# Performance work log

Hardware: AMD Instinct MI355X
Metric: run time of the kernel (lower is better)

The kernel has to match this reference:

```python
import jax, jax.numpy as jnp
import numpy as np
import itertools, math

METRIC = [1.0, 1.0, 1.0]  # Cl(3,0)
EPS = 1e-6
SQRT2 = math.sqrt(2.0)


def _build_algebra(metric):
    d = len(metric)
    # basis blades ordered by grade, then lexicographic combination (repo convention)
    blades = []
    for g in range(d + 1):
        for c in itertools.combinations(range(d), g):
            blades.append(sum(1 << i for i in c))
    idx = {m: i for i, m in enumerate(blades)}
    n = len(blades)
    C = np.zeros((n, n, n), dtype=np.float32)  # cayley[i, j, k]: e_i * e_k -> sign * e_j
    for ia, am in enumerate(blades):
        for ik, bm in enumerate(blades):
            a = am >> 1
            swaps = 0
            while a:
                swaps += bin(a & bm).count('1')
                a >>= 1
            sign = -1.0 if (swaps & 1) else 1.0
            for i in range(d):
                if am & bm & (1 << i):
                    sign *= metric[i]
            C[ia, idx[am ^ bm], ik] = sign
    grades = np.array([bin(m).count('1') for m in blades])
    subspaces = np.array([int((grades == g).sum()) for g in range(d + 1)])
    paths = np.zeros((d + 1, d + 1, d + 1), dtype=bool)
    for i in range(d + 1):
        for j in range(d + 1):
            for k in range(d + 1):
                paths[i, j, k] = np.any(C[np.ix_(grades == i, grades == j, grades == k)] != 0)
    return C, subspaces, paths, grades

CAYLEY_NP, SUBSPACES, PATHS, GRADE_OF_COMP = _build_algebra(METRIC)
REP_IDX = np.repeat(np.arange(len(SUBSPACES)), SUBSPACES)  # component -> grade, len 8
PI, PJ, PK = np.nonzero(PATHS)                              # 20 active grade triples
ONEHOT_GRADE = np.eye(len(SUBSPACES), dtype=np.float32)[GRADE_OF_COMP]  # [8,4]

B, N_IN, N_OUT = 1024, 256, 256
DIM_MV = CAYLEY_NP.shape[0]  # 8
N_PATHS = int(PATHS.sum())   # 20


def mv_linear(x, w, bias=None):
    # MVLinear: per-grade weight repeated over components; einsum 'bm...i,nmi->bn...i'
    wr = w[:, :, REP_IDX]                       # [out, in, 8]
    out = jnp.einsum('bmi,nmi->bni', x, wr)
    if bias is not None:
        out = out.at[:, :, 0].add(bias[:, :, 0])  # bias embedded in scalar (grade-0) slot
    return out


def normalize_mv(x, a):
    # per-grade norms (Euclidean metric => L2 norm of each grade block)
    oh = jnp.asarray(ONEHOT_GRADE)
    norms = jnp.sqrt(jnp.einsum('bni,ig->bng', x * x, oh))  # [b, n, 4]
    interp = jax.nn.sigmoid(a)[None] * (norms - 1.0) + 1.0  # learned interp toward unit norm
    return x / (interp[:, :, REP_IDX] + EPS)


def gp_kernel(gp_weight):
    # scatter 20 path weights into (m, n, 4, 4, 4), repeat per subspace, mask by cayley
    m, n, _ = gp_weight.shape
    g = len(SUBSPACES)
    w4 = jnp.zeros((m, n, g, g, g), gp_weight.dtype).at[:, :, PI, PJ, PK].set(gp_weight)
    wrep = w4[:, :, REP_IDX][:, :, :, REP_IDX][:, :, :, :, REP_IDX]  # [m, n, 8, 8, 8]
    return jnp.asarray(CAYLEY_NP)[None, None] * wrep


def setup_inputs() -> dict:
    key = jax.random.key(0)
    ks = jax.random.split(key, 5)
    std_gp = 1.0 / math.sqrt(N_IN * (len(METRIC) + 1))
    std_lin = 1.0 / math.sqrt(N_IN)
    return {
        'x': jax.random.normal(ks[0], (B, N_IN, DIM_MV), jnp.float32),
        'w_right': jax.random.normal(ks[1], (N_IN, N_IN, len(SUBSPACES)), jnp.float32) * std_lin,
        'w_left': jax.random.normal(ks[2], (N_OUT, N_IN, len(SUBSPACES)), jnp.float32) * std_lin,
        'b_left': jax.random.normal(ks[3], (1, N_OUT, 1), jnp.float32) * 0.02,
        'norm_a': jnp.zeros((N_IN, len(SUBSPACES)), jnp.float32),  # normalization_init = 0
        'gp_weight': jax.random.normal(ks[4], (N_OUT, N_IN, N_PATHS), jnp.float32) * std_gp,
    }


def reference(x, w_right, w_left, b_left, norm_a, gp_weight):
    x_right = normalize_mv(mv_linear(x, w_right), norm_a)
    kernel = gp_kernel(gp_weight)                 # [m, n, 8, 8, 8]
    outer = jnp.einsum('bni,bnk->bnik', x, x_right)  # [b, n, 8, 8]
    prod = jnp.einsum('bnik,mnijk->bmj', outer, kernel)
    left = mv_linear(x, w_left, b_left)
    return (left + prod) / SQRT2
```

## Files before the change

### kernel.cpp

```cpp
#include <hip/hip_runtime.h>
#include <math.h>

typedef unsigned short ushortT;
typedef __bf16 bf16x8 __attribute__((ext_vector_type(8)));
typedef float  f32x4  __attribute__((ext_vector_type(4)));

__constant__ int GRADEc[8] = {0,1,1,1,2,2,2,3};

__constant__ int CMAPc[8][7] = {
  {0, 8, 9,10,11, 0, 0},
  {1,12,13,14,15,16,17},
  {2,18,19,20,21,22,23},
  {3,24,25,26,27,28,29},
  {4,30,31,32,33,34,35},
  {5,36,37,38,39,40,41},
  {6,42,43,44,45,46,47},
  {7,48,49,50,51, 0, 0}};
__constant__ int WMAPc[8][7] = {
  {0, 4, 8,14,20, 0, 0},
  {1, 5, 9,10,15,16,21},
  {1, 5, 9,10,15,16,21},
  {1, 5, 9,10,15,16,21},
  {2, 6,11,12,17,18,22},
  {2, 6,11,12,17,18,22},
  {2, 6,11,12,17,18,22},
  {3, 7,13,19,23, 0, 0}};
__constant__ int SSTARTc[8][4] = {
  {0,2,3,4},{0,2,4,6},{0,2,4,6},{0,2,4,6},
  {0,2,4,6},{0,2,4,6},{0,2,4,6},{0,2,3,4}};
__constant__ int SCOUNTc[8][4] = {
  {2,1,1,1},{2,2,2,1},{2,2,2,1},{2,2,2,1},
  {2,2,2,1},{2,2,2,1},{2,2,2,1},{2,1,1,1}};

__device__ __forceinline__ ushortT f2bf(float f) {
  unsigned int u = __float_as_uint(f);
  unsigned int r = (u + 0x7fffu + ((u >> 16) & 1u)) >> 16;
  return (ushortT)r;
}

__global__ void k_transpose_x(const float* __restrict__ x, float* __restrict__ xT) {
  __shared__ float tile[32][33];
  int c0 = blockIdx.x * 32;
  int b0 = blockIdx.y * 32;
  int tx = threadIdx.x & 31, ty = threadIdx.x >> 5;
  #pragma unroll
  for (int i = 0; i < 32; i += 8)
    tile[ty + i][tx] = x[(b0 + ty + i) * 2048 + c0 + tx];
  __syncthreads();
  #pragma unroll
  for (int i = 0; i < 32; i += 8)
    xT[(c0 + ty + i) * 1024 + b0 + tx] = tile[tx][ty + i];
}

__global__ void k_build_wr(const float* __restrict__ w_right, float* __restrict__ WR) {
  int t = blockIdx.x * 256 + threadIdx.x;
  int n = t & 255, m = (t >> 8) & 255, g = t >> 16;
  WR[t] = w_right[n * 1024 + m * 4 + g];
}

__global__ void k_build_wt2(const float* __restrict__ w_left, const float* __restrict__ gp,
                            ushortT* __restrict__ WT2b) {
  int t = blockIdx.x * 256 + threadIdx.x;
  int n = t & 255, m = (t >> 8) & 255, w = t >> 16;
  float v;
  if (w < 4)       v = w_left[m * 1024 + n * 4 + w];
  else             v = gp[m * 5120 + n * 20 + (w - 4)];
  WT2b[t] = f2bf(v);
}

__global__ __launch_bounds__(256) void k_gemm_right2(const float* __restrict__ WR,
                                                     const float* __restrict__ xT,
                                                     float* __restrict__ y2) {
  const int i  = blockIdx.z;
  const int g  = GRADEc[i];
  const int b0 = blockIdx.y * 64;
  const int n0 = blockIdx.x * 64;
  __shared__ float sX[32 * 64];
  __shared__ float sW[32 * 64];
  const int t  = threadIdx.x;
  const int tx = t & 15, ty = t >> 4;
  float acc[4][4] = {};
  const float* Xbase = xT + i * 1024 + b0;
  const float* Wbase = WR + g * 65536 + n0;
  for (int k0 = 0; k0 < 256; k0 += 32) {
    int col = t & 63, krow = t >> 6;
    #pragma unroll
    for (int l = 0; l < 8; ++l) {
      int kk = krow + l * 4;
      sX[kk * 64 + col] = Xbase[(k0 + kk) * 8192 + col];
      sW[kk * 64 + col] = Wbase[(k0 + kk) * 256 + col];
    }
    __syncthreads();
    #pragma unroll
    for (int kk = 0; kk < 32; ++kk) {
      const float4 a = *(const float4*)(sX + kk * 64 + (ty << 2));
      const float4 w = *(const float4*)(sW + kk * 64 + (tx << 2));
      float ar[4] = {a.x, a.y, a.z, a.w};
      float wr4[4] = {w.x, w.y, w.z, w.w};
      #pragma unroll
      for (int r = 0; r < 4; ++r)
        #pragma unroll
        for (int c = 0; c < 4; ++c)
          acc[r][c] = fmaf(ar[r], wr4[c], acc[r][c]);
    }
    __syncthreads();
  }
  #pragma unroll
  for (int r = 0; r < 4; ++r) {
    float4 v = make_float4(acc[r][0], acc[r][1], acc[r][2], acc[r][3]);
    *(float4*)(y2 + i * 262144 + (b0 + (ty << 2) + r) * 256 + n0 + (tx << 2)) = v;
  }
}

__global__ void k_features2(const float* __restrict__ y2, const float* __restrict__ x,
                            const float* __restrict__ norm_a, ushortT* __restrict__ FT2b) {
  const int b = blockIdx.x;
  const int n = threadIdx.x;
  float y[8], xv[8];
  #pragma unroll
  for (int i = 0; i < 8; ++i) y[i] = y2[i * 262144 + b * 256 + n];
  const float4* xp = (const float4*)(x + b * 2048 + n * 8);
  float4 x01 = xp[0], x23 = xp[1];
  xv[0]=x01.x; xv[1]=x01.y; xv[2]=x01.z; xv[3]=x01.w;
  xv[4]=x23.x; xv[5]=x23.y; xv[6]=x23.z; xv[7]=x23.w;
  float4 na = *(const float4*)(norm_a + n * 4);
  float nav[4] = {na.x, na.y, na.z, na.w};
  float nr[4];
  nr[0] = fabsf(y[0]);
  nr[1] = sqrtf(y[1]*y[1] + y[2]*y[2] + y[3]*y[3]);
  nr[2] = sqrtf(y[4]*y[4] + y[5]*y[5] + y[6]*y[6]);
  nr[3] = fabsf(y[7]);
  float inv[4];
  #pragma unroll
  for (int g = 0; g < 4; ++g) {
    float s = 1.0f / (1.0f + expf(-nav[g]));
    inv[g] = 1.0f / (s * (nr[g] - 1.0f) + 1.0f + 1e-6f);
  }
  float r[8];
  r[0] = y[0]*inv[0];
  r[1] = y[1]*inv[1]; r[2] = y[2]*inv[1]; r[3] = y[3]*inv[1];
  r[4] = y[4]*inv[2]; r[5] = y[5]*inv[2]; r[6] = y[6]*inv[2];
  r[7] = y[7]*inv[3];

  float F[52];
  #pragma unroll
  for (int i = 0; i < 8; ++i) F[i] = xv[i];
  F[8]  = xv[0]*r[0];
  F[9]  = xv[1]*r[1] + xv[2]*r[2] + xv[3]*r[3];
  F[10] = -(xv[4]*r[4] + xv[5]*r[5] + xv[6]*r[6]);
  F[11] = -xv[7]*r[7];
  F[12] = xv[0]*r[1];
  F[13] = xv[1]*r[0];
  F[14] = -(xv[2]*r[4] + xv[3]*r[5]);
  F[15] = xv[4]*r[2] + xv[5]*r[3];
  F[16] = -xv[6]*r[7];
  F[17] = -xv[7]*r[6];
  F[18] = xv[0]*r[2];
  F[19] = xv[2]*r[0];
  F[20] = xv[1]*r[4] - xv[3]*r[6];
  F[21] = -xv[4]*r[1] + xv[6]*r[3];
  F[22] = xv[5]*r[7];
  F[23] = xv[7]*r[5];
  F[24] = xv[0]*r[3];
  F[25] = xv[3]*r[0];
  F[26] = xv[1]*r[5] + xv[2]*r[6];
  F[27] = -(xv[5]*r[1] + xv[6]*r[2]);
  F[28] = -xv[4]*r[7];
  F[29] = -xv[7]*r[4];
  F[30] = xv[0]*r[4];
  F[31] = xv[1]*r[2] - xv[2]*r[1];
  F[32] = xv[3]*r[7];
  F[33] = xv[4]*r[0];
  F[34] = -xv[5]*r[6] + xv[6]*r[5];
  F[35] = xv[7]*r[3];
  F[36] = xv[0]*r[5];
  F[37] = xv[1]*r[3] - xv[3]*r[1];
  F[38] = -xv[2]*r[7];
  F[39] = xv[5]*r[0];
  F[40] = xv[4]*r[6] - xv[6]*r[4];
  F[41] = -xv[7]*r[2];
  F[42] = xv[0]*r[6];
  F[43] = xv[2]*r[3] - xv[3]*r[2];
  F[44] = xv[1]*r[7];
  F[45] = xv[6]*r[0];
  F[46] = -xv[4]*r[5] + xv[5]*r[4];
  F[47] = xv[7]*r[1];
  F[48] = xv[0]*r[7];
  F[49] = xv[1]*r[6] - xv[2]*r[5] + xv[3]*r[4];
  F[50] = xv[4]*r[3] - xv[5]*r[2] + xv[6]*r[1];
  F[51] = xv[7]*r[0];

  #pragma unroll
  for (int c = 0; c < 52; ++c)
    FT2b[c * 262144 + b * 256 + n] = f2bf(F[c]);
}

__global__ __launch_bounds__(256) void k_gemm_mfma(const ushortT* __restrict__ FT2b,
                                                   const ushortT* __restrict__ WT2b,
                                                   float* __restrict__ outP) {
  const int j  = blockIdx.z >> 2;
  const int ks = blockIdx.z & 3;
  const int b0 = blockIdx.y * 128;
  const int m0 = blockIdx.x * 128;
  __shared__ ushortT sA[128 * 40];
  __shared__ ushortT sB[128 * 40];
  const int t    = threadIdx.x;
  const int wave = t >> 6;
  const int lane = t & 63;
  const int wb   = (wave & 1) * 64;
  const int wm   = (wave >> 1) * 64;
  const int lrow = lane & 15;
  const int lkg  = lane >> 4;

  f32x4 acc[4][4];
  #pragma unroll
  for (int r = 0; r < 4; ++r)
    #pragma unroll
    for (int c = 0; c < 4; ++c)
      acc[r][c] = (f32x4){0.f, 0.f, 0.f, 0.f};

  const int row0 = t >> 2, seg0 = t & 3;
  const int row1 = (t + 256) >> 2, seg1 = t & 3;

  const int sstart = SSTARTc[j][ks];
  const int scnt   = SCOUNTc[j][ks];
  for (int s2 = 0; s2 < scnt; ++s2) {
    const int slot = sstart + s2;
    const ushortT* Ap = FT2b + CMAPc[j][slot] * 262144 + b0 * 256;
    const ushortT* Bp = WT2b + WMAPc[j][slot] * 65536 + m0 * 256;
    for (int n0 = 0; n0 < 256; n0 += 32) {
      uint4 va0 = *(const uint4*)(Ap + row0 * 256 + n0 + seg0 * 8);
      uint4 vb0 = *(const uint4*)(Bp + row0 * 256 + n0 + seg0 * 8);
      uint4 va1 = *(const uint4*)(Ap + row1 * 256 + n0 + seg1 * 8);
      uint4 vb1 = *(const uint4*)(Bp + row1 * 256 + n0 + seg1 * 8);
      *(uint4*)(sA + row0 * 40 + seg0 * 8) = va0;
      *(uint4*)(sB + row0 * 40 + seg0 * 8) = vb0;
      *(uint4*)(sA + row1 * 40 + seg1 * 8) = va1;
      *(uint4*)(sB + row1 * 40 + seg1 * 8) = vb1;
      __syncthreads();
      bf16x8 af[4], bf[4];
      #pragma unroll
      for (int r = 0; r < 4; ++r)
        af[r] = *(const bf16x8*)(sA + (wb + r * 16 + lrow) * 40 + lkg * 8);
      #pragma unroll
      for (int c = 0; c < 4; ++c)
        bf[c] = *(const bf16x8*)(sB + (wm + c * 16 + lrow) * 40 + lkg * 8);
      #pragma unroll
      for (int r = 0; r < 4; ++r)
        #pragma unroll
        for (int c = 0; c < 4; ++c)
          acc[r][c] = __builtin_amdgcn_mfma_f32_16x16x32_bf16(af[r], bf[c], acc[r][c], 0, 0, 0);
      __syncthreads();
    }
  }

  float* oj = outP + (ks * 8 + j) * 262144;
  #pragma unroll
  for (int r = 0; r < 4; ++r) {
    #pragma unroll
    for (int c = 0; c < 4; ++c) {
      #pragma unroll
      for (int e = 0; e < 4; ++e) {
        int brow = b0 + wb + r * 16 + lkg * 4 + e;
        int mcol = m0 + wm + c * 16 + lrow;
        oj[brow * 256 + mcol] = acc[r][c][e];
      }
    }
  }
}

__global__ void k_merge(const float* __restrict__ outP, const float* __restrict__ bleft,
                        float* __restrict__ out) {
  const int idx = blockIdx.x * 256 + threadIdx.x;
  const int m = idx & 255;
  const float bias = bleft[m];
  const float sc = 0.7071067811865475f;
  float o[8];
  #pragma unroll
  for (int jj = 0; jj < 8; ++jj) {
    float s = 0.0f;
    #pragma unroll
    for (int p = 0; p < 4; ++p)
      s += outP[(p * 8 + jj) * 262144 + idx];
    o[jj] = s;
  }
  o[0] += bias;
  float4 v0 = make_float4(o[0]*sc, o[1]*sc, o[2]*sc, o[3]*sc);
  float4 v1 = make_float4(o[4]*sc, o[5]*sc, o[6]*sc, o[7]*sc);
  *(float4*)(out + idx * 8)     = v0;
  *(float4*)(out + idx * 8 + 4) = v1;
}

extern "C" void kernel_launch(void* const* d_in, const int* in_sizes, int n_in,
                              void* d_out, int out_size, void* d_ws, size_t ws_size,
                              hipStream_t stream) {
  const float* x       = (const float*)d_in[0];
  const float* w_right = (const float*)d_in[1];
  const float* w_left  = (const float*)d_in[2];
  const float* b_left  = (const float*)d_in[3];
  const float* norm_a  = (const float*)d_in[4];
  const float* gp      = (const float*)d_in[5];
  float* out = (float*)d_out;
  float* W   = (float*)d_ws;

  float*   xT   = W;
  float*   WR   = W + 2097152;
  float*   y2   = W + 2359296;
  float*   outP = W + 4456448;
  ushortT* FT2b = (ushortT*)(W + 12845056);
  ushortT* WT2b = (ushortT*)(W + 19660800);

  k_transpose_x<<<dim3(64, 32), 256, 0, stream>>>(x, xT);
  k_build_wr<<<1024, 256, 0, stream>>>(w_right, WR);
  k_build_wt2<<<6144, 256, 0, stream>>>(w_left, gp, WT2b);
  k_gemm_right2<<<dim3(4, 16, 8), 256, 0, stream>>>(WR, xT, y2);
  k_features2<<<1024, 256, 0, stream>>>(y2, x, norm_a, FT2b);
  k_gemm_mfma<<<dim3(2, 8, 32), 256, 0, stream>>>(FT2b, WT2b, outP);
  k_merge<<<1024, 256, 0, stream>>>(outP, b_left, out);
}
```

Baseline: 136.0 us.

## Move right-side linear to split-bf16 MFMA and use direct-to-LDS swizzled loads

```diff
diff --git a/kernel.cpp b/kernel.cpp
--- a/kernel.cpp
+++ b/kernel.cpp
@@ -38,24 +38,39 @@
   return (ushortT)r;
 }
 
-__global__ void k_transpose_x(const float* __restrict__ x, float* __restrict__ xT) {
-  __shared__ float tile[32][33];
-  int c0 = blockIdx.x * 32;
-  int b0 = blockIdx.y * 32;
-  int tx = threadIdx.x & 31, ty = threadIdx.x >> 5;
-  #pragma unroll
-  for (int i = 0; i < 32; i += 8)
-    tile[ty + i][tx] = x[(b0 + ty + i) * 2048 + c0 + tx];
-  __syncthreads();
-  #pragma unroll
-  for (int i = 0; i < 32; i += 8)
-    xT[(c0 + ty + i) * 1024 + b0 + tx] = tile[tx][ty + i];
-}
-
-__global__ void k_build_wr(const float* __restrict__ w_right, float* __restrict__ WR) {
-  int t = blockIdx.x * 256 + threadIdx.x;
-  int n = t & 255, m = (t >> 8) & 255, g = t >> 16;
-  WR[t] = w_right[n * 1024 + m * 4 + g];
+#define GLOAD_LDS16(gsrc, ldst) \
+  __builtin_amdgcn_global_load_lds((const __attribute__((address_space(1))) unsigned int*)(gsrc), \
+                                   (__attribute__((address_space(3))) unsigned int*)(ldst), 16, 0, 0)
+
+__global__ void k_xsplit(const float* __restrict__ x, ushortT* __restrict__ XH,
+                         ushortT* __restrict__ XL) {
+  const int b = blockIdx.x;
+  const int m = threadIdx.x;
+  const float4* xp = (const float4*)(x + b * 2048 + m * 8);
+  float4 a = xp[0], c = xp[1];
+  float v[8] = {a.x, a.y, a.z, a.w, c.x, c.y, c.z, c.w};
+  #pragma unroll
+  for (int i = 0; i < 8; ++i) {
+    ushortT h = f2bf(v[i]);
+    float hf = __uint_as_float(((unsigned int)h) << 16);
+    XH[i * 262144 + b * 256 + m] = h;
+    XL[i * 262144 + b * 256 + m] = f2bf(v[i] - hf);
+  }
+}
+
+__global__ void k_wsplit(const float* __restrict__ w_right, ushortT* __restrict__ WH,
+                         ushortT* __restrict__ WL) {
+  const int n = blockIdx.x;
+  const int m = threadIdx.x;
+  float4 w = *(const float4*)(w_right + n * 1024 + m * 4);
+  float v[4] = {w.x, w.y, w.z, w.w};
+  #pragma unroll
+  for (int g = 0; g < 4; ++g) {
+    ushortT h = f2bf(v[g]);
+    float hf = __uint_as_float(((unsigned int)h) << 16);
+    WH[g * 65536 + n * 256 + m] = h;
+    WL[g * 65536 + n * 256 + m] = f2bf(v[g] - hf);
+  }
 }
 
 __global__ void k_build_wt2(const float* __restrict__ w_left, const float* __restrict__ gp,
@@ -68,48 +83,82 @@
   WT2b[t] = f2bf(v);
 }
 
-__global__ __launch_bounds__(256) void k_gemm_right2(const float* __restrict__ WR,
-                                                     const float* __restrict__ xT,
-                                                     float* __restrict__ y2) {
+__global__ __launch_bounds__(256) void k_right_mfma(const ushortT* __restrict__ XH,
+                                                    const ushortT* __restrict__ XL,
+                                                    const ushortT* __restrict__ WH,
+                                                    const ushortT* __restrict__ WL,
+                                                    float* __restrict__ y2) {
   const int i  = blockIdx.z;
   const int g  = GRADEc[i];
   const int b0 = blockIdx.y * 64;
   const int n0 = blockIdx.x * 64;
-  __shared__ float sX[32 * 64];
-  __shared__ float sW[32 * 64];
-  const int t  = threadIdx.x;
-  const int tx = t & 15, ty = t >> 4;
-  float acc[4][4] = {};
-  const float* Xbase = xT + i * 1024 + b0;
-  const float* Wbase = WR + g * 65536 + n0;
+  __shared__ __align__(16) ushortT lds[4 * 2048];
+  const int t = threadIdx.x;
+  const int wave = t >> 6, lane = t & 63;
+  const int wb = (wave & 1) * 32, wn = (wave >> 1) * 32;
+  const int lrow = lane & 15, lkg = lane >> 4;
+
+  const ushortT* Ah = XH + i * 262144 + b0 * 256;
+  const ushortT* Al = XL + i * 262144 + b0 * 256;
+  const ushortT* Bh = WH + g * 65536 + n0 * 256;
+  const ushortT* Bl = WL + g * 65536 + n0 * 256;
+  const ushortT* gp0 = (wave == 0) ? Ah : (wave == 1) ? Al : (wave == 2) ? Bh : Bl;
+  ushortT* lbase = lds + wave * 2048;
+
+  const int srow = lane >> 2;
+  const int sseg = lane & 3;
+
+  f32x4 acc[2][2];
+  #pragma unroll
+  for (int r = 0; r < 2; ++r)
+    #pragma unroll
+    for (int c = 0; c < 2; ++c)
+      acc[r][c] = (f32x4){0.f, 0.f, 0.f, 0.f};
+
   for (int k0 = 0; k0 < 256; k0 += 32) {
-    int col = t & 63, krow = t >> 6;
-    #pragma unroll
-    for (int l = 0; l < 8; ++l) {
-      int kk = krow + l * 4;
-      sX[kk * 64 + col] = Xbase[(k0 + kk) * 8192 + col];
-      sW[kk * 64 + col] = Wbase[(k0 + kk) * 256 + col];
+    #pragma unroll
+    for (int q = 0; q < 4; ++q) {
+      int row = q * 16 + srow;
+      int slog = sseg ^ ((row >> 1) & 3);
+      GLOAD_LDS16(gp0 + row * 256 + k0 + slog * 8, lbase + q * 512);
     }
     __syncthreads();
-    #pragma unroll
-    for (int kk = 0; kk < 32; ++kk) {
-      const float4 a = *(const float4*)(sX + kk * 64 + (ty << 2));
-      const float4 w = *(const float4*)(sW + kk * 64 + (tx << 2));
-      float ar[4] = {a.x, a.y, a.z, a.w};
-      float wr4[4] = {w.x, w.y, w.z, w.w};
-      #pragma unroll
-      for (int r = 0; r < 4; ++r)
-        #pragma unroll
-        for (int c = 0; c < 4; ++c)
-          acc[r][c] = fmaf(ar[r], wr4[c], acc[r][c]);
-    }
+    bf16x8 afh[2], afl[2], bfh[2], bfl[2];
+    #pragma unroll
+    for (int r = 0; r < 2; ++r) {
+      int row = wb + r * 16 + lrow;
+      int po = row * 32 + (lkg ^ ((row >> 1) & 3)) * 8;
+      afh[r] = *(const bf16x8*)(lds + po);
+      afl[r] = *(const bf16x8*)(lds + 2048 + po);
+    }
+    #pragma unroll
+    for (int c = 0; c < 2; ++c) {
+      int row = wn + c * 16 + lrow;
+      int po = row * 32 + (lkg ^ ((row >> 1) & 3)) * 8;
+      bfh[c] = *(const bf16x8*)(lds + 4096 + po);
+      bfl[c] = *(const bf16x8*)(lds + 6144 + po);
+    }
+    #pragma unroll
+    for (int r = 0; r < 2; ++r)
+      #pragma unroll
+      for (int c = 0; c < 2; ++c) {
+        acc[r][c] = __builtin_amdgcn_mfma_f32_16x16x32_bf16(afh[r], bfh[c], acc[r][c], 0, 0, 0);
+        acc[r][c] = __builtin_amdgcn_mfma_f32_16x16x32_bf16(afl[r], bfh[c], acc[r][c], 0, 0, 0);
+        acc[r][c] = __builtin_amdgcn_mfma_f32_16x16x32_bf16(afh[r], bfl[c], acc[r][c], 0, 0, 0);
+      }
     __syncthreads();
   }
-  #pragma unroll
-  for (int r = 0; r < 4; ++r) {
-    float4 v = make_float4(acc[r][0], acc[r][1], acc[r][2], acc[r][3]);
-    *(float4*)(y2 + i * 262144 + (b0 + (ty << 2) + r) * 256 + n0 + (tx << 2)) = v;
-  }
+
+  #pragma unroll
+  for (int r = 0; r < 2; ++r)
+    #pragma unroll
+    for (int c = 0; c < 2; ++c)
+      #pragma unroll
+      for (int e = 0; e < 4; ++e) {
+        int brow = b0 + wb + r * 16 + lkg * 4 + e;
+        int ncol = n0 + wn + c * 16 + lrow;
+        y2[i * 262144 + brow * 256 + ncol] = acc[r][c][e];
+      }
 }
 
 __global__ void k_features2(const float* __restrict__ y2, const float* __restrict__ x,
@@ -143,8 +192,6 @@
   r[7] = y[7]*inv[3];
 
   float F[52];
-  #pragma unroll
-  for (int i = 0; i < 8; ++i) F[i] = xv[i];
   F[8]  = xv[0]*r[0];
   F[9]  = xv[1]*r[1] + xv[2]*r[2] + xv[3]*r[3];
   F[10] = -(xv[4]*r[4] + xv[5]*r[5] + xv[6]*r[6]);
@@ -191,19 +238,20 @@
   F[51] = xv[7]*r[0];
 
   #pragma unroll
-  for (int c = 0; c < 52; ++c)
+  for (int c = 8; c < 52; ++c)
     FT2b[c * 262144 + b * 256 + n] = f2bf(F[c]);
 }
 
-__global__ __launch_bounds__(256) void k_gemm_mfma(const ushortT* __restrict__ FT2b,
+__global__ __launch_bounds__(256) void k_gemm_mfma(const ushortT* __restrict__ XH,
+                                                   const ushortT* __restrict__ FT2b,
                                                    const ushortT* __restrict__ WT2b,
                                                    float* __restrict__ outP) {
   const int j  = blockIdx.z >> 2;
   const int ks = blockIdx.z & 3;
   const int b0 = blockIdx.y * 128;
   const int m0 = blockIdx.x * 128;
-  __shared__ ushortT sA[128 * 40];
-  __shared__ ushortT sB[128 * 40];
+  __shared__ __align__(16) ushortT sA[128 * 64];
+  __shared__ __align__(16) ushortT sB[128 * 64];
   const int t    = threadIdx.x;
   const int wave = t >> 6;
   const int lane = t & 63;
@@ -211,6 +259,8 @@
   const int wm   = (wave >> 1) * 64;
   const int lrow = lane & 15;
   const int lkg  = lane >> 4;
+  const int srow = lane >> 3;
+  const int sseg = lane & 7;
 
   f32x4 acc[4][4];
   #pragma unroll
@@ -218,38 +268,43 @@
     #pragma unroll
     for (int c = 0; c < 4; ++c)
       acc[r][c] = (f32x4){0.f, 0.f, 0.f, 0.f};
-
-  const int row0 = t >> 2, seg0 = t & 3;
-  const int row1 = (t + 256) >> 2, seg1 = t & 3;
 
   const int sstart = SSTARTc[j][ks];
   const int scnt   = SCOUNTc[j][ks];
   for (int s2 = 0; s2 < scnt; ++s2) {
     const int slot = sstart + s2;
-    const ushortT* Ap = FT2b + CMAPc[j][slot] * 262144 + b0 * 256;
+    const ushortT* Ap = ((slot == 0) ? (XH + j * 262144)
+                                     : (FT2b + CMAPc[j][slot] * 262144)) + b0 * 256;
     const ushortT* Bp = WT2b + WMAPc[j][slot] * 65536 + m0 * 256;
-    for (int n0 = 0; n0 < 256; n0 += 32) {
-      uint4 va0 = *(const uint4*)(Ap + row0 * 256 + n0 + seg0 * 8);
-      uint4 vb0 = *(const uint4*)(Bp + row0 * 256 + n0 + seg0 * 8);
-      uint4 va1 = *(const uint4*)(Ap + row1 * 256 + n0 + seg1 * 8);
-      uint4 vb1 = *(const uint4*)(Bp + row1 * 256 + n0 + seg1 * 8);
-      *(uint4*)(sA + row0 * 40 + seg0 * 8) = va0;
-      *(uint4*)(sB + row0 * 40 + seg0 * 8) = vb0;
-      *(uint4*)(sA + row1 * 40 + seg1 * 8) = va1;
-      *(uint4*)(sB + row1 * 40 + seg1 * 8) = vb1;
+    for (int k0 = 0; k0 < 256; k0 += 64) {
+      #pragma unroll
+      for (int q = 0; q < 4; ++q) {
+        int idx = wave * 4 + q;
+        int row = idx * 8 + srow;
+        int slog = sseg ^ (row & 7);
+        GLOAD_LDS16(Ap + row * 256 + k0 + slog * 8, sA + idx * 512);
+        GLOAD_LDS16(Bp + row * 256 + k0 + slog * 8, sB + idx * 512);
+      }
       __syncthreads();
-      bf16x8 af[4], bf[4];
-      #pragma unroll
-      for (int r = 0; r < 4; ++r)
-        af[r] = *(const bf16x8*)(sA + (wb + r * 16 + lrow) * 40 + lkg * 8);
-      #pragma unroll
-      for (int c = 0; c < 4; ++c)
-        bf[c] = *(const bf16x8*)(sB + (wm + c * 16 + lrow) * 40 + lkg * 8);
-      #pragma unroll
-      for (int r = 0; r < 4; ++r)
+      #pragma unroll
+      for (int kk = 0; kk < 2; ++kk) {
+        bf16x8 af[4], bf[4];
         #pragma unroll
-        for (int c = 0; c < 4; ++c)
-          acc[r][c] = __builtin_amdgcn_mfma_f32_16x16x32_bf16(af[r], bf[c], acc[r][c], 0, 0, 0);
+        for (int r = 0; r < 4; ++r) {
+          int row = wb + r * 16 + lrow;
+          af[r] = *(const bf16x8*)(sA + row * 64 + (((kk * 4 + lkg) ^ (row & 7)) * 8));
+        }
+        #pragma unroll
+        for (int c = 0; c < 4; ++c) {
+          int row = wm + c * 16 + lrow;
+          bf[c] = *(const bf16x8*)(sB + row * 64 + (((kk * 4 + lkg) ^ (row & 7)) * 8));
+        }
+        #pragma unroll
+        for (int r = 0; r < 4; ++r)
+          #pragma unroll
+          for (int c = 0; c < 4; ++c)
+            acc[r][c] = __builtin_amdgcn_mfma_f32_16x16x32_bf16(af[r], bf[c], acc[r][c], 0, 0, 0);
+      }
       __syncthreads();
     }
   }
@@ -303,18 +358,20 @@
   float* out = (float*)d_out;
   float* W   = (float*)d_ws;
 
-  float*   xT   = W;
-  float*   WR   = W + 2097152;
-  float*   y2   = W + 2359296;
-  float*   outP = W + 4456448;
+  float*   y2   = W;
+  float*   outP = W + 2097152;
+  ushortT* XH   = (ushortT*)(W + 10485760);
+  ushortT* XL   = (ushortT*)(W + 11534336);
+  ushortT* WH   = (ushortT*)(W + 12582912);
+  ushortT* WL   = (ushortT*)(W + 12713984);
   ushortT* FT2b = (ushortT*)(W + 12845056);
   ushortT* WT2b = (ushortT*)(W + 19660800);
 
-  k_transpose_x<<<dim3(64, 32), 256, 0, stream>>>(x, xT);
-  k_build_wr<<<1024, 256, 0, stream>>>(w_right, WR);
+  k_xsplit<<<1024, 256, 0, stream>>>(x, XH, XL);
+  k_wsplit<<<256, 256, 0, stream>>>(w_right, WH, WL);
   k_build_wt2<<<6144, 256, 0, stream>>>(w_left, gp, WT2b);
-  k_gemm_right2<<<dim3(4, 16, 8), 256, 0, stream>>>(WR, xT, y2);
+  k_right_mfma<<<dim3(4, 16, 8), 256, 0, stream>>>(XH, XL, WH, WL, y2);
   k_features2<<<1024, 256, 0, stream>>>(y2, x, norm_a, FT2b);
-  k_gemm_mfma<<<dim3(2, 8, 32), 256, 0, stream>>>(FT2b, WT2b, outP);
+  k_gemm_mfma<<<dim3(2, 8, 32), 256, 0, stream>>>(XH, FT2b, WT2b, outP);
   k_merge<<<1024, 256, 0, stream>>>(outP, b_left, out);
 }
```

After: 121.0 us. -11.0%, faster.
